# Kernel optimization log

Hardware: AMD Instinct MI355X
Metric: run time of the kernel (lower is better)

The kernel has to match this reference:

```python
import jax, jax.numpy as jnp
import numpy as np

B, S, HID = 2, 2048, 4096
H, P, N, G, K = 128, 64, 128, 8, 4      # heads, head_dim, ssm_state, groups, conv kernel
INTER = H * P                           # 8192
CONV_DIM = INTER + 2 * G * N            # 10240
CHUNK = 128
EPS = 1e-5
DT_MIN, DT_MAX = 0.0, 100.0


def setup_inputs() -> dict:
    key = jax.random.key(0)
    ks = jax.random.split(key, 4)
    proj = INTER + CONV_DIM + H
    return {
        "x": jax.random.normal(ks[0], (B, S, HID), jnp.float32),
        "in_proj_w": jax.random.normal(ks[1], (proj, HID), jnp.float32) * 0.02,
        "conv_w": jax.random.normal(ks[2], (CONV_DIM, 1, K), jnp.float32) * 0.2,
        "conv_b": jnp.zeros((CONV_DIM,), jnp.float32),
        "dt_bias": jnp.ones((H,), jnp.float32),
        "A_log": jnp.log(jnp.arange(1, H + 1, dtype=jnp.float32)),
        "D": jnp.ones((H,), jnp.float32),
        "norm_w": jnp.ones((INTER,), jnp.float32),
        "out_proj_w": jax.random.normal(ks[3], (HID, INTER), jnp.float32) * 0.02,
    }


def _segsum(a):
    # a: (..., c) -> (..., c, c); [i, j] = sum_{k=j+1..i} a[k] for i >= j, else -inf
    c = a.shape[-1]
    s = jnp.cumsum(a, axis=-1)
    diff = s[..., :, None] - s[..., None, :]
    mask = jnp.tril(jnp.ones((c, c), dtype=bool))
    return jnp.where(mask, diff, -jnp.inf)


def reference(x, in_proj_w, conv_w, conv_b, dt_bias, A_log, D, norm_w, out_proj_w):
    b, s, _ = x.shape
    proj = jnp.einsum('bsd,ed->bse', x, in_proj_w)
    gate = proj[..., :INTER]
    hBC = proj[..., INTER:INTER + CONV_DIM]
    dt = proj[..., INTER + CONV_DIM:]                       # (b, s, H)

    # depthwise causal conv1d + silu
    xc = jnp.transpose(hBC, (0, 2, 1))                      # (b, conv_dim, s)
    xc = jax.lax.conv_general_dilated(xc, conv_w, (1,), [(K - 1, 0)],
                                      dimension_numbers=('NCH', 'OIH', 'NCH'),
                                      feature_group_count=CONV_DIM)
    xc = xc + conv_b[None, :, None]
    hBC = jax.nn.silu(jnp.transpose(xc, (0, 2, 1)))

    hs = hBC[..., :INTER].reshape(b, s, H, P)
    Bm = hBC[..., INTER:INTER + G * N].reshape(b, s, G, N)
    Cm = hBC[..., INTER + G * N:].reshape(b, s, G, N)

    A = -jnp.exp(A_log)                                     # (H,)
    dt = jnp.clip(jax.nn.softplus(dt + dt_bias), DT_MIN, DT_MAX)

    rep = H // G
    Bh = jnp.repeat(Bm, rep, axis=2)                        # (b, s, H, N)
    Ch = jnp.repeat(Cm, rep, axis=2)

    nc = s // CHUNK
    xch = (hs * dt[..., None]).reshape(b, nc, CHUNK, H, P)  # dt-scaled input, chunked
    Bc = Bh.reshape(b, nc, CHUNK, H, N)
    Cc = Ch.reshape(b, nc, CHUNK, H, N)
    A_dt = (dt * A).reshape(b, nc, CHUNK, H).transpose(0, 3, 1, 2)  # (b, H, nc, c)
    A_cum = jnp.cumsum(A_dt, axis=-1)

    # intra-chunk (diagonal) contribution
    L = jnp.exp(_segsum(A_dt))                              # (b, H, nc, c, c)
    Y_diag = jnp.einsum('bzlhn,bzshn,bhzls,bzshp->bzlhp', Cc, Bc, L, xch)

    # per-chunk final states
    decay_states = jnp.exp(A_cum[..., -1:] - A_cum)         # (b, H, nc, c)
    states = jnp.einsum('bzlhn,bhzl,bzlhp->bzhpn', Bc, decay_states, xch)

    # inter-chunk recurrence (initial state = 0)
    states_p = jnp.concatenate([jnp.zeros_like(states[:, :1]), states], axis=1)  # (b, nc+1, H, P, N)
    A_last = jnp.pad(A_cum[..., -1], ((0, 0), (0, 0), (1, 0)))                   # (b, H, nc+1)
    decay_chunk = jnp.exp(_segsum(A_last))                                        # (b, H, nc+1, nc+1)
    new_states = jnp.einsum('bhzc,bchpn->bzhpn', decay_chunk, states_p)
    prev = new_states[:, :-1]                                # state entering each chunk

    Y_off = jnp.einsum('bzlhn,bzhpn,bhzl->bzlhp', Cc, prev, jnp.exp(A_cum))
    Y = (Y_diag + Y_off).reshape(b, s, H, P) + hs * D[None, None, :, None]
    y = Y.reshape(b, s, INTER)

    # gated grouped RMSNorm (norm_before_gate=False)
    g = y * jax.nn.silu(gate)
    gg = g.reshape(b, s, G, INTER // G)
    var = jnp.mean(gg * gg, axis=-1, keepdims=True)
    gg = gg * jax.lax.rsqrt(var + EPS)
    out = gg.reshape(b, s, INTER) * norm_w

    return jnp.einsum('bsi,oi->bso', out, out_proj_w)
```

## Files before the change

### kernel.cpp

```cpp
#include <hip/hip_runtime.h>
#include <hip/hip_bf16.h>
#include <cstdint>
#include <cstddef>

#define DEVI __device__ __forceinline__

#define BB 2
#define S_LEN 2048
#define HID_DIM 4096
#define NH 128
#define PD 64
#define NS 128
#define NG 8
#define INTER 8192
#define CONVD 10240
#define PROJ 18560
#define PROJP 18688
#define NC 16
#define BS 4096
#define GN 1024

using short8 = __attribute__((ext_vector_type(8))) short;
using short4v = __attribute__((ext_vector_type(4))) short;
using f32x4  = __attribute__((ext_vector_type(4))) float;
using bf16x8 = __attribute__((ext_vector_type(8))) __bf16;

DEVI float bf2f(short u) {
  union { unsigned int i; float f; } v;
  v.i = ((unsigned int)(unsigned short)u) << 16;
  return v.f;
}
DEVI short f2bf(float f) {
  union { float ff; unsigned int i; } v; v.ff = f;
  unsigned int x = v.i;
  return (short)((x + 0x7fffu + ((x >> 16) & 1u)) >> 16);
}
DEVI f32x4 mfma16(short8 a, short8 b, f32x4 c) {
  return __builtin_amdgcn_mfma_f32_16x16x32_bf16(
      __builtin_bit_cast(bf16x8, a), __builtin_bit_cast(bf16x8, b), c, 0, 0, 0);
}
DEVI void gl_lds16(const short* g, short* l) {
  __builtin_amdgcn_global_load_lds(
      (const __attribute__((address_space(1))) void*)g,
      (__attribute__((address_space(3))) void*)l, 16, 0, 0);
}
DEVI float sigmoidf_(float x) { return 1.f / (1.f + __expf(-x)); }

__global__ __launch_bounds__(256) void cvt_f32_bf16_k(const float* __restrict__ in,
                                                      short* __restrict__ out, size_t n) {
  size_t i = ((size_t)blockIdx.x * 256 + threadIdx.x) * 8;
  if (i + 8 > n) return;
  float4 a = *(const float4*)(in + i);
  float4 b = *(const float4*)(in + i + 4);
  short8 o;
  o[0] = f2bf(a.x); o[1] = f2bf(a.y); o[2] = f2bf(a.z); o[3] = f2bf(a.w);
  o[4] = f2bf(b.x); o[5] = f2bf(b.y); o[6] = f2bf(b.z); o[7] = f2bf(b.w);
  *(short8*)(out + i) = o;
}


#define STG(ISB, BUF, KH, TILE) do { \
  const short* _src = (ISB) ? Bt : A; \
  const int _r0 = (ISB) ? n0 : m0; \
  short* _lb = lds_ + ((ISB) ? 32768 : 0) + ((BUF)*2+(KH))*8192; \
  const int _kt = (TILE)*64 + (KH)*32; \
  { int _row = (wid*2)*16 + srow; int _sl = sps ^ ((_row>>1)&3); \
    gl_lds16(_src + (size_t)(_r0+_row)*K + _kt + _sl*8, _lb + (wid*2)*512); } \
  { int _row = (wid*2+1)*16 + srow; int _sl = sps ^ ((_row>>1)&3); \
    gl_lds16(_src + (size_t)(_r0+_row)*K + _kt + _sl*8, _lb + (wid*2+1)*512); } \
} while(0)

#define NOPS ((void)0)
#define VM6 asm volatile("s_waitcnt vmcnt(6)" ::: "memory")
#define VM0 asm volatile("s_waitcnt vmcnt(0)" ::: "memory")

#define LDAF(DST, BUF, KH, MIH) do { \
  _Pragma("unroll") \
  for (int _m = 0; _m < 4; ++_m) { \
    int _row = wr*128 + ((MIH)*4+_m)*16 + fr; \
    DST[_m] = *(const short8*)(lds_ + ((BUF)*2+(KH))*8192 + _row*32 + ((slot ^ ((_row>>1)&3))<<3)); \
  } \
} while(0)

#define LDBF(DST, BUF, KH) do { \
  _Pragma("unroll") \
  for (int _n = 0; _n < 4; ++_n) { \
    int _row = wc*64 + _n*16 + fr; \
    DST[_n] = *(const short8*)(lds_ + 32768 + ((BUF)*2+(KH))*8192 + _row*32 + ((slot ^ ((_row>>1)&3))<<3)); \
  } \
} while(0)

#define PH2(CAF, CBF, MIH, PFEN, PFAF, PFBF, PFB, PFKH, PFMIH, PFDOB, STGS, VMW) do { \
  STGS; VMW; \
  __builtin_amdgcn_s_barrier(); \
  if (PFEN) { LDAF(PFAF, PFB, PFKH, PFMIH); if (PFDOB) LDBF(PFBF, PFB, PFKH); } \
  __builtin_amdgcn_s_setprio(1); \
  _Pragma("unroll") \
  for (int _m = 0; _m < 4; ++_m) \
    _Pragma("unroll") \
    for (int _n = 0; _n < 4; ++_n) \
      acc[(MIH)*4+_m][_n] = mfma16(CAF[_m], CBF[_n], acc[(MIH)*4+_m][_n]); \
  __builtin_amdgcn_s_setprio(0); \
  asm volatile("s_waitcnt lgkmcnt(0)" ::: "memory"); \
  __builtin_amdgcn_sched_barrier(0); \
  __builtin_amdgcn_s_barrier(); \
} while(0)

template<int CB16>
__global__ __launch_bounds__(512, 2) void gemm256_k(const short* __restrict__ A,
                                                    const short* __restrict__ Bt,
                                                    void* __restrict__ Cout,
                                                    int Nstride, int K, int ntn) {
  __shared__ short lds_[65536];
  const int tid = threadIdx.x, wid = tid >> 6, lane = tid & 63;
  const int nwg = gridDim.x, orig = blockIdx.x;
  const int swz = (orig & 7) * (nwg >> 3) + (orig >> 3);
  const int per_group = ntn << 3;
  const int group = swz / per_group;
  const int rem = swz - group * per_group;
  const int m0 = (group * 8 + (rem & 7)) * 256;
  const int n0 = (rem >> 3) * 256;
  const int wr = wid >> 2, wc = wid & 3;
  const int fr = lane & 15, slot = lane >> 4;
  const int srow = lane >> 2, sps = lane & 3;

  f32x4 acc[8][4] = {};
  short8 af_a[4], af_b[4], bf_a[4], bf_b[4];
  const int NT = K >> 6;

  STG(1, 0, 0, 0); STG(0, 0, 0, 0); STG(1, 0, 1, 0); STG(0, 0, 1, 0);
  asm volatile("s_waitcnt vmcnt(4)" ::: "memory");
  STG(1, 1, 0, 1); STG(0, 1, 0, 1); STG(1, 1, 1, 1);
  asm volatile("s_waitcnt vmcnt(6)" ::: "memory");
  __builtin_amdgcn_s_barrier();
  LDAF(af_a, 0, 0, 0); LDBF(bf_a, 0, 0);
  asm volatile("s_waitcnt lgkmcnt(0)" ::: "memory");
  __builtin_amdgcn_sched_barrier(0);

  for (int i = 0; i < (NT >> 1) - 1; ++i) {
    const int t = 2 * i;
    PH2(af_a, bf_a, 0, 1, af_b, bf_a, 0, 0, 1, 0, STG(0, 1, 1, t + 1), NOPS);
    PH2(af_b, bf_a, 1, 1, af_a, bf_b, 0, 1, 0, 1, STG(1, 0, 0, t + 2), NOPS);
    PH2(af_a, bf_b, 0, 1, af_b, bf_a, 0, 1, 1, 0, STG(0, 0, 0, t + 2), NOPS);
    PH2(af_b, bf_b, 1, 1, af_a, bf_a, 1, 0, 0, 1, STG(1, 0, 1, t + 2), VM6);
    PH2(af_a, bf_a, 0, 1, af_b, bf_b, 1, 0, 1, 0, STG(0, 0, 1, t + 2), NOPS);
    PH2(af_b, bf_a, 1, 1, af_a, bf_b, 1, 1, 0, 1, STG(1, 1, 0, t + 3), NOPS);
    PH2(af_a, bf_b, 0, 1, af_b, bf_a, 1, 1, 1, 0, STG(0, 1, 0, t + 3), NOPS);
    PH2(af_b, bf_b, 1, 1, af_a, bf_a, 0, 0, 0, 1, STG(1, 1, 1, t + 3), VM6);
  }
  PH2(af_a, bf_a, 0, 1, af_b, bf_a, 0, 0, 1, 0, STG(0, 1, 1, NT - 1), NOPS);
  PH2(af_b, bf_a, 1, 1, af_a, bf_b, 0, 1, 0, 1, NOPS, NOPS);
  PH2(af_a, bf_b, 0, 1, af_b, bf_a, 0, 1, 1, 0, NOPS, NOPS);
  PH2(af_b, bf_b, 1, 1, af_a, bf_a, 1, 0, 0, 1, NOPS, VM0);
  PH2(af_a, bf_a, 0, 1, af_b, bf_b, 1, 0, 1, 0, NOPS, NOPS);
  PH2(af_b, bf_a, 1, 1, af_a, bf_b, 1, 1, 0, 1, NOPS, NOPS);
  PH2(af_a, bf_b, 0, 1, af_b, bf_a, 1, 1, 1, 0, NOPS, NOPS);
  PH2(af_b, bf_b, 1, 0, af_a, bf_a, 0, 0, 0, 0, NOPS, NOPS);

  const int er = (lane >> 4) * 4, ec = lane & 15;
  if (CB16) {
    short* C = (short*)Cout;
#pragma unroll
    for (int mi = 0; mi < 8; ++mi)
#pragma unroll
      for (int j = 0; j < 4; ++j) {
        size_t base = (size_t)(m0 + wr * 128 + mi * 16 + er + j) * Nstride + n0 + wc * 64 + ec;
#pragma unroll
        for (int ni = 0; ni < 4; ++ni) C[base + ni * 16] = f2bf(acc[mi][ni][j]);
      }
  } else {
    float* C = (float*)Cout;
#pragma unroll
    for (int mi = 0; mi < 8; ++mi)
#pragma unroll
      for (int j = 0; j < 4; ++j) {
        size_t base = (size_t)(m0 + wr * 128 + mi * 16 + er + j) * Nstride + n0 + wc * 64 + ec;
#pragma unroll
        for (int ni = 0; ni < 4; ++ni) C[base + ni * 16] = acc[mi][ni][j];
      }
  }
}

__global__ __launch_bounds__(256) void conv_silu_k(const short* __restrict__ projb,
                                                   const float* __restrict__ convw,
                                                   const float* __restrict__ convb,
                                                   short* __restrict__ hbc) {
  const int c = blockIdx.x * 256 + threadIdx.x;
  const int s0 = blockIdx.y * 256;
  const int b = blockIdx.z;
  const size_t rb = (size_t)b * S_LEN;
  const float* wp = convw + (size_t)c * 4;
  const float w0 = wp[0], w1 = wp[1], w2 = wp[2], w3 = wp[3];
  const float bias = convb[c];
  const short* pcol = projb + INTER + c;
  float x1 = 0.f, x2 = 0.f, x3 = 0.f;
  if (s0 > 0) {
    x3 = bf2f(pcol[(rb + s0 - 3) * PROJP]);
    x2 = bf2f(pcol[(rb + s0 - 2) * PROJP]);
    x1 = bf2f(pcol[(rb + s0 - 1) * PROJP]);
  }
  for (int s = s0; s < s0 + 256; ++s) {
    float v = bf2f(pcol[(rb + s) * PROJP]);
    float acc = bias + w0 * x3 + w1 * x2 + w2 * x1 + w3 * v;
    float o = acc * sigmoidf_(acc);
    hbc[(rb + s) * CONVD + c] = f2bf(o);
    x3 = x2; x2 = x1; x1 = v;
  }
}

__global__ __launch_bounds__(128) void acum_k(const short* __restrict__ projb,
                                              const float* __restrict__ dt_bias,
                                              const float* __restrict__ A_log,
                                              float* __restrict__ dtT,
                                              float* __restrict__ acum) {
  const int l = threadIdx.x;
  const int z = blockIdx.x, h = blockIdx.y, b = blockIdx.z;
  const float A = -__expf(A_log[h]);
  __shared__ float sv[128];
  const int r = b * S_LEN + z * 128 + l;
  float xv = bf2f(projb[(size_t)r * PROJP + INTER + CONVD + h]) + dt_bias[h];
  float sp = (xv > 20.f) ? xv : log1pf(__expf(xv));
  sp = fminf(fmaxf(sp, 0.f), 100.f);
  const size_t base = ((size_t)(b * NH + h)) * S_LEN + z * 128;
  dtT[base + l] = sp;
  sv[l] = sp * A;
  __syncthreads();
  for (int off = 1; off < 128; off <<= 1) {
    float t = (l >= off) ? sv[l - off] : 0.f;
    __syncthreads();
    sv[l] += t;
    __syncthreads();
  }
  acum[base + l] = sv[l];
}

__global__ __launch_bounds__(512) void states_k(const short* __restrict__ hbc,
                                                const float* __restrict__ dtT,
                                                const float* __restrict__ acum,
                                                float* __restrict__ states) {
  __shared__ short sBT[128 * 128];
  __shared__ short sxdt[64 * 128];
  const int tid = threadIdx.x, wid = tid >> 6, lane = tid & 63;
  const int g = blockIdx.x, z = blockIdx.y, b = blockIdx.z;
  const size_t srow0 = (size_t)(b * S_LEN + z * 128);
  const short* hrow = hbc + srow0 * CONVD;

  {
    const int l = tid & 127, n0b = (tid >> 7) * 32;
    const short* src = hrow + (size_t)l * CONVD + INTER + g * NS + n0b;
    short8 v0 = *(const short8*)(src);
    short8 v1 = *(const short8*)(src + 8);
    short8 v2 = *(const short8*)(src + 16);
    short8 v3 = *(const short8*)(src + 24);
#pragma unroll
    for (int j = 0; j < 8; ++j) {
      sBT[(n0b + j) * 128 + l] = v0[j];
      sBT[(n0b + 8 + j) * 128 + l] = v1[j];
      sBT[(n0b + 16 + j) * 128 + l] = v2[j];
      sBT[(n0b + 24 + j) * 128 + l] = v3[j];
    }
  }

  const int fr = lane & 15, fk8 = (lane >> 4) * 8;
  const int er = (lane >> 4) * 4, ec = lane & 15;
  const int pband = (wid & 3) * 16, nhalf = (wid >> 2) * 64;
  const int s2 = tid & 63, p0w = (tid >> 6) * 8;
  unsigned int* sx32 = (unsigned int*)sxdt;

  for (int hh = 0; hh < 16; ++hh) {
    const int h = g * 16 + hh;
    const float* ac_g = acum + ((size_t)(b * NH + h)) * S_LEN + z * 128;
    const float* dts = dtT + ((size_t)(b * NH + h)) * S_LEN + z * 128;
    __syncthreads();
    {
      const float acL = ac_g[127];
      float dv0 = dts[2 * s2] * __expf(acL - ac_g[2 * s2]);
      float dv1 = dts[2 * s2 + 1] * __expf(acL - ac_g[2 * s2 + 1]);
      const short* rsrc = hrow + (size_t)(2 * s2) * CONVD + (size_t)h * PD + p0w;
      short8 r0 = *(const short8*)(rsrc);
      short8 r1 = *(const short8*)(rsrc + CONVD);
#pragma unroll
      for (int j = 0; j < 8; ++j) {
        unsigned int lo = (unsigned short)f2bf(bf2f(r0[j]) * dv0);
        unsigned int hi = (unsigned short)f2bf(bf2f(r1[j]) * dv1);
        sx32[(p0w + j) * 64 + s2] = lo | (hi << 16);
      }
    }
    __syncthreads();
    f32x4 st[4] = {};
#pragma unroll
    for (int kk = 0; kk < 4; ++kk) {
      short8 a = *(const short8*)(sxdt + (pband + fr) * 128 + kk * 32 + fk8);
#pragma unroll
      for (int ni = 0; ni < 4; ++ni) {
        short8 bb = *(const short8*)(sBT + (nhalf + ni * 16 + fr) * 128 + kk * 32 + fk8);
        st[ni] = mfma16(a, bb, st[ni]);
      }
    }
    float* stp = states + (((size_t)(b * NC + z)) * NH + h) * (size_t)(NS * PD);
#pragma unroll
    for (int ni = 0; ni < 4; ++ni)
#pragma unroll
      for (int j = 0; j < 4; ++j)
        stp[(pband + er + j) * NS + nhalf + ni * 16 + ec] = st[ni][j];
  }
}

__global__ __launch_bounds__(256) void scan_k(float* __restrict__ states,
                                              const float* __restrict__ acum) {
  const int h = blockIdx.x, b = blockIdx.y;
  const int tid = threadIdx.x;
  float* stp = states + ((size_t)(b * NC * NH) + h) * (size_t)(NS * PD);
  const size_t cst = (size_t)NH * NS * PD;
  const float* ac = acum + ((size_t)(b * NH + h)) * S_LEN;
  float E[32];
#pragma unroll
  for (int i = 0; i < 32; ++i) E[i] = 0.f;
  const int n = tid & 127, pg = tid >> 7;
  for (int zz = 0; zz < NC; ++zz) {
    float* sz = stp + (size_t)zz * cst;
    short* pvb = (short*)sz;
    float tmp[32];
#pragma unroll
    for (int i = 0; i < 32; ++i) tmp[i] = sz[i * 256 + tid];
    __syncthreads();
    float dec = __expf(ac[zz * 128 + 127]);
#pragma unroll
    for (int i = 0; i < 32; ++i) {
      int p = i * 2 + pg;
      pvb[p * 128 + n] = f2bf(E[i]);
      E[i] = dec * E[i] + tmp[i];
    }
    __syncthreads();
  }
}

__global__ __launch_bounds__(512) void yfull_k(const short* __restrict__ hbc,
                                               const short* __restrict__ projb,
                                               const float* __restrict__ dtT,
                                               const float* __restrict__ acum,
                                               const float* __restrict__ states,
                                               const float* __restrict__ Dv,
                                               const float* __restrict__ norm_w,
                                               short* __restrict__ normed) {
  __shared__ short lds[50176];
  __shared__ float sac[128];
  __shared__ float sScale[128];
  __shared__ float sNW[1024];
  short* sC = lds;
  short* sB = lds + 16384;
  short* sxdt = lds + 16384;
  short* sprev = lds + 16384 + 8192;
  const int tid = threadIdx.x, wid = tid >> 6, lane = tid & 63;
  short* sPw = lds + 32768 + wid * 2176;
  const int g = blockIdx.x, z = blockIdx.y, b = blockIdx.z;
  const size_t srow0 = (size_t)(b * S_LEN + z * 128);
  const short* hrow = hbc + srow0 * CONVD;

  {
    const int n0_ = (lane & 15) * 8;
#pragma unroll
    for (int it = 0; it < 4; ++it) {
      int s = it * 32 + wid * 4 + (lane >> 4);
      gl_lds16(hrow + (size_t)s * CONVD + INTER + GN + g * NS + n0_, sC + (it * 32 + wid * 4) * 128);
      gl_lds16(hrow + (size_t)s * CONVD + INTER + g * NS + n0_, sB + (it * 32 + wid * 4) * 128);
    }
  }
  for (int i = tid; i < 1024; i += 512) sNW[i] = norm_w[g * 1024 + i];
  __syncthreads();

  const int fr = lane & 15, fk8 = (lane >> 4) * 8;
  const int er = (lane >> 4) * 4, ec = lane & 15;
  const int lrow = wid * 16;
  const int s2 = tid & 63, p0w = (tid >> 6) * 8;
  unsigned int* sx32 = (unsigned int*)sxdt;

  f32x4 sc[8] = {};
#pragma unroll
  for (int kk = 0; kk < 4; ++kk) {
    short8 a = *(const short8*)(sC + (lrow + fr) * 128 + kk * 32 + fk8);
#pragma unroll
    for (int si = 0; si < 8; ++si) {
      short8 bv = *(const short8*)(sB + (si * 16 + fr) * 128 + kk * 32 + fk8);
      sc[si] = mfma16(a, bv, sc[si]);
    }
  }

  float rssq[4] = {0.f, 0.f, 0.f, 0.f};

  for (int hh = 0; hh < 16; ++hh) {
    const int h = g * 16 + hh;
    const float* ac = acum + ((size_t)(b * NH + h)) * S_LEN + z * 128;
    const float* dts = dtT + ((size_t)(b * NH + h)) * S_LEN + z * 128;
    const short* pvb = (const short*)(states + (((size_t)(b * NC + z)) * NH + h) * (size_t)(NS * PD));
    __syncthreads();
    if (tid < 128) sac[tid] = ac[tid];
    {
      float dv0 = dts[2 * s2], dv1 = dts[2 * s2 + 1];
      const short* rsrc = hrow + (size_t)(2 * s2) * CONVD + (size_t)h * PD + p0w;
      short8 r0 = *(const short8*)(rsrc);
      short8 r1 = *(const short8*)(rsrc + CONVD);
#pragma unroll
      for (int j = 0; j < 8; ++j) {
        unsigned int lo = (unsigned short)f2bf(bf2f(r0[j]) * dv0);
        unsigned int hi = (unsigned short)f2bf(bf2f(r1[j]) * dv1);
        sx32[(p0w + j) * 64 + s2] = lo | (hi << 16);
      }
    }
    gl_lds16(pvb + wid * 1024 + lane * 8, sprev + wid * 1024);
    gl_lds16(pvb + wid * 1024 + 512 + lane * 8, sprev + wid * 1024 + 512);
    __syncthreads();

    {
      float acS[8];
#pragma unroll
      for (int si = 0; si < 8; ++si) acS[si] = sac[si * 16 + ec];
#pragma unroll
      for (int j = 0; j < 4; ++j) {
        int lloc = er + j;
        float acl = sac[lrow + lloc];
#pragma unroll
        for (int si = 0; si < 8; ++si) {
          int s = si * 16 + ec;
          float v = (s <= lrow + lloc) ? sc[si][j] * __expf(acl - acS[si]) : 0.f;
          sPw[lloc * 136 + s] = f2bf(v);
        }
      }
    }
    f32x4 yd[4] = {}, yo[4] = {};
#pragma unroll
    for (int kk = 0; kk < 4; ++kk) {
      short8 ap = *(const short8*)(sPw + fr * 136 + kk * 32 + fk8);
      short8 acf = *(const short8*)(sC + (lrow + fr) * 128 + kk * 32 + fk8);
#pragma unroll
      for (int ni = 0; ni < 4; ++ni) {
        short8 bv = *(const short8*)(sxdt + (ni * 16 + fr) * 128 + kk * 32 + fk8);
        yd[ni] = mfma16(ap, bv, yd[ni]);
        short8 bp = *(const short8*)(sprev + (ni * 16 + fr) * 128 + kk * 32 + fk8);
        yo[ni] = mfma16(acf, bp, yo[ni]);
      }
    }
    const float Dh = Dv[h];
#pragma unroll
    for (int j = 0; j < 4; ++j) {
      int l = lrow + er + j;
      float e_ac = __expf(sac[l]);
#pragma unroll
      for (int ni = 0; ni < 4; ++ni) {
        int p = ni * 16 + ec;
        float hs = bf2f(hrow[(size_t)l * CONVD + (size_t)h * PD + p]);
        float y = yd[ni][j] + yo[ni][j] * e_ac + hs * Dh;
        float gate = bf2f(projb[(srow0 + l) * (size_t)PROJP + (size_t)h * PD + p]);
        float gg = y * gate * sigmoidf_(gate);
        normed[(srow0 + l) * (size_t)INTER + (size_t)h * PD + p] = f2bf(gg);
        rssq[j] += gg * gg;
      }
    }
  }

#pragma unroll
  for (int j = 0; j < 4; ++j) {
#pragma unroll
    for (int m = 1; m <= 8; m <<= 1) rssq[j] += __shfl_xor(rssq[j], m, 64);
  }
  if (ec == 0) {
#pragma unroll
    for (int j = 0; j < 4; ++j) sScale[lrow + er + j] = rsqrtf(rssq[j] * (1.f / 1024.f) + 1e-5f);
  }
  __syncthreads();

  for (int e = tid * 8; e < 128 * 1024; e += 4096) {
    int row = e >> 10, ch = e & 1023;
    short* gp = normed + (srow0 + row) * (size_t)INTER + g * 1024 + ch;
    short8 gv = *(const short8*)(gp);
    float scl = sScale[row];
    short8 o;
#pragma unroll
    for (int q = 0; q < 8; ++q) o[q] = f2bf(bf2f(gv[q]) * scl * sNW[ch + q]);
    *(short8*)(gp) = o;
  }
}

extern "C" void kernel_launch(void* const* d_in, const int* in_sizes, int n_in,
                              void* d_out, int out_size, void* d_ws, size_t ws_size,
                              hipStream_t stream) {
  const float* x     = (const float*)d_in[0];
  const float* w1    = (const float*)d_in[1];
  const float* convw = (const float*)d_in[2];
  const float* convb = (const float*)d_in[3];
  const float* dtb   = (const float*)d_in[4];
  const float* alog  = (const float*)d_in[5];
  const float* Dv    = (const float*)d_in[6];
  const float* nw    = (const float*)d_in[7];
  const float* w2    = (const float*)d_in[8];
  float* out = (float*)d_out;

  char* ws = (char*)d_ws;
  size_t off = 0;
  float* dtT = (float*)(ws + off);  off += (size_t)BB * NH * S_LEN * 4;
  float* acum = (float*)(ws + off); off += (size_t)BB * NH * S_LEN * 4;
  short* xb = (short*)(ws + off);   off += (size_t)BS * HID_DIM * 2;
  char* w1region = ws + off;        off += (size_t)PROJP * HID_DIM * 2;
  short* w1b = (short*)w1region;
  short* normed = (short*)w1region;
  short* w2b = (short*)(w1region + (size_t)BS * INTER * 2);
  short* projb = (short*)(ws + off); off += (size_t)BS * PROJP * 2;
  short* hbc = (short*)(ws + off);   off += (size_t)BS * CONVD * 2;
  float* states = (float*)(ws + off); off += (size_t)BB * NC * NH * NS * PD * 4;

  const size_t nx = (size_t)BS * HID_DIM;
  const size_t nw1 = (size_t)PROJ * HID_DIM;
  const size_t nw2 = (size_t)HID_DIM * INTER;

  cvt_f32_bf16_k<<<dim3(nx / 2048), 256, 0, stream>>>(x, xb, nx);
  cvt_f32_bf16_k<<<dim3(nw1 / 2048), 256, 0, stream>>>(w1, w1b, nw1);

  gemm256_k<1><<<dim3(16 * 73), 512, 0, stream>>>(xb, w1b, projb, PROJP, HID_DIM, 73);

  cvt_f32_bf16_k<<<dim3(nw2 / 2048), 256, 0, stream>>>(w2, w2b, nw2);

  conv_silu_k<<<dim3(CONVD / 256, S_LEN / 256, BB), 256, 0, stream>>>(projb, convw, convb, hbc);
  acum_k<<<dim3(NC, NH, BB), 128, 0, stream>>>(projb, dtb, alog, dtT, acum);

  states_k<<<dim3(NG, NC, BB), 512, 0, stream>>>(hbc, dtT, acum, states);
  scan_k<<<dim3(NH, BB), 256, 0, stream>>>(states, acum);
  yfull_k<<<dim3(NG, NC, BB), 512, 0, stream>>>(hbc, projb, dtT, acum, states, Dv, nw, normed);

  gemm256_k<0><<<dim3(16 * 16), 512, 0, stream>>>(normed, w2b, out, HID_DIM, INTER, 16);
}
```

Baseline: 1.250 ms.

## Double-buffer per-head staging and swizzle LDS in states and y kernels

In states_k and yfull_k, the global loads for the next head (x*dt, acum, dt, prev states) are issued into registers before the current head's MFMA work. They are then written into the alternate LDS buffer afterward, which drops one barrier per head and overlaps load latency with compute. LDS layouts are padded (stride 136) or XOR-swizzled to reduce bank conflicts, and acum values move from shared memory into registers. The cost is more LDS (yfull grows to about 133KB) and higher register pressure, which could lower occupancy.

```diff
diff --git a/kernel.cpp b/kernel.cpp
--- a/kernel.cpp
+++ b/kernel.cpp
@@ -57,7 +57,6 @@
   o[4] = f2bf(b.x); o[5] = f2bf(b.y); o[6] = f2bf(b.z); o[7] = f2bf(b.w);
   *(short8*)(out + i) = o;
 }
-
 
 #define STG(ISB, BUF, KH, TILE) do { \
   const short* _src = (ISB) ? Bt : A; \
@@ -238,8 +237,8 @@
                                                 const float* __restrict__ dtT,
                                                 const float* __restrict__ acum,
                                                 float* __restrict__ states) {
-  __shared__ short sBT[128 * 128];
-  __shared__ short sxdt[64 * 128];
+  __shared__ short sBT[128 * 136];
+  __shared__ short sxdt2[2][64 * 136];
   const int tid = threadIdx.x, wid = tid >> 6, lane = tid & 63;
   const int g = blockIdx.x, z = blockIdx.y, b = blockIdx.z;
   const size_t srow0 = (size_t)(b * S_LEN + z * 128);
@@ -254,10 +253,10 @@
     short8 v3 = *(const short8*)(src + 24);
 #pragma unroll
     for (int j = 0; j < 8; ++j) {
-      sBT[(n0b + j) * 128 + l] = v0[j];
-      sBT[(n0b + 8 + j) * 128 + l] = v1[j];
-      sBT[(n0b + 16 + j) * 128 + l] = v2[j];
-      sBT[(n0b + 24 + j) * 128 + l] = v3[j];
+      sBT[(n0b + j) * 136 + l] = v0[j];
+      sBT[(n0b + 8 + j) * 136 + l] = v1[j];
+      sBT[(n0b + 16 + j) * 136 + l] = v2[j];
+      sBT[(n0b + 24 + j) * 136 + l] = v3[j];
     }
   }
 
@@ -265,35 +264,52 @@
   const int er = (lane >> 4) * 4, ec = lane & 15;
   const int pband = (wid & 3) * 16, nhalf = (wid >> 2) * 64;
   const int s2 = tid & 63, p0w = (tid >> 6) * 8;
-  unsigned int* sx32 = (unsigned int*)sxdt;
+
+  float cdv0, cdv1; short8 cr0, cr1;
+  {
+    const int h = g * 16;
+    const float* acg = acum + ((size_t)(b * NH + h)) * S_LEN + z * 128;
+    const float* dts = dtT + ((size_t)(b * NH + h)) * S_LEN + z * 128;
+    const float acL = acg[127];
+    cdv0 = dts[2 * s2] * __expf(acL - acg[2 * s2]);
+    cdv1 = dts[2 * s2 + 1] * __expf(acL - acg[2 * s2 + 1]);
+    const short* rsrc = hrow + (size_t)(2 * s2) * CONVD + (size_t)h * PD + p0w;
+    cr0 = *(const short8*)(rsrc);
+    cr1 = *(const short8*)(rsrc + CONVD);
+  }
+  {
+    unsigned int* x32 = (unsigned int*)sxdt2[0];
+#pragma unroll
+    for (int j = 0; j < 8; ++j) {
+      unsigned int lo = (unsigned short)f2bf(bf2f(cr0[j]) * cdv0);
+      unsigned int hi = (unsigned short)f2bf(bf2f(cr1[j]) * cdv1);
+      x32[(p0w + j) * 68 + s2] = lo | (hi << 16);
+    }
+  }
+  __syncthreads();
 
   for (int hh = 0; hh < 16; ++hh) {
     const int h = g * 16 + hh;
-    const float* ac_g = acum + ((size_t)(b * NH + h)) * S_LEN + z * 128;
-    const float* dts = dtT + ((size_t)(b * NH + h)) * S_LEN + z * 128;
-    __syncthreads();
-    {
-      const float acL = ac_g[127];
-      float dv0 = dts[2 * s2] * __expf(acL - ac_g[2 * s2]);
-      float dv1 = dts[2 * s2 + 1] * __expf(acL - ac_g[2 * s2 + 1]);
-      const short* rsrc = hrow + (size_t)(2 * s2) * CONVD + (size_t)h * PD + p0w;
-      short8 r0 = *(const short8*)(rsrc);
-      short8 r1 = *(const short8*)(rsrc + CONVD);
-#pragma unroll
-      for (int j = 0; j < 8; ++j) {
-        unsigned int lo = (unsigned short)f2bf(bf2f(r0[j]) * dv0);
-        unsigned int hi = (unsigned short)f2bf(bf2f(r1[j]) * dv1);
-        sx32[(p0w + j) * 64 + s2] = lo | (hi << 16);
-      }
-    }
-    __syncthreads();
+    float ndv0 = 0.f, ndv1 = 0.f; short8 nr0, nr1;
+    if (hh < 15) {
+      const int h2 = h + 1;
+      const float* acg = acum + ((size_t)(b * NH + h2)) * S_LEN + z * 128;
+      const float* dts = dtT + ((size_t)(b * NH + h2)) * S_LEN + z * 128;
+      const float acL = acg[127];
+      ndv0 = dts[2 * s2] * __expf(acL - acg[2 * s2]);
+      ndv1 = dts[2 * s2 + 1] * __expf(acL - acg[2 * s2 + 1]);
+      const short* rsrc = hrow + (size_t)(2 * s2) * CONVD + (size_t)h2 * PD + p0w;
+      nr0 = *(const short8*)(rsrc);
+      nr1 = *(const short8*)(rsrc + CONVD);
+    }
+    const short* sx = sxdt2[hh & 1];
     f32x4 st[4] = {};
 #pragma unroll
     for (int kk = 0; kk < 4; ++kk) {
-      short8 a = *(const short8*)(sxdt + (pband + fr) * 128 + kk * 32 + fk8);
+      short8 a = *(const short8*)(sx + (pband + fr) * 136 + kk * 32 + fk8);
 #pragma unroll
       for (int ni = 0; ni < 4; ++ni) {
-        short8 bb = *(const short8*)(sBT + (nhalf + ni * 16 + fr) * 128 + kk * 32 + fk8);
+        short8 bb = *(const short8*)(sBT + (nhalf + ni * 16 + fr) * 136 + kk * 32 + fk8);
         st[ni] = mfma16(a, bb, st[ni]);
       }
     }
@@ -303,6 +319,16 @@
 #pragma unroll
       for (int j = 0; j < 4; ++j)
         stp[(pband + er + j) * NS + nhalf + ni * 16 + ec] = st[ni][j];
+    if (hh < 15) {
+      unsigned int* x32 = (unsigned int*)sxdt2[(hh + 1) & 1];
+#pragma unroll
+      for (int j = 0; j < 8; ++j) {
+        unsigned int lo = (unsigned short)f2bf(bf2f(nr0[j]) * ndv0);
+        unsigned int hi = (unsigned short)f2bf(bf2f(nr1[j]) * ndv1);
+        x32[(p0w + j) * 68 + s2] = lo | (hi << 16);
+      }
+    }
+    __syncthreads();
   }
 }
 
@@ -335,6 +361,39 @@
   }
 }
 
+#define RDSW(BUF, ROWBASE, KK) \
+  (*(const short8*)((BUF) + ((ROWBASE) + fr) * 128 + ((((KK) * 4 + slot4) ^ sw7) << 3)))
+
+#define WRX(DST, D0, D1, R0, R1) do { \
+  unsigned int* _x = (unsigned int*)(DST); \
+  _Pragma("unroll") \
+  for (int _j = 0; _j < 8; ++_j) { \
+    unsigned int _lo = (unsigned short)f2bf(bf2f(R0[_j]) * (D0)); \
+    unsigned int _hi = (unsigned short)f2bf(bf2f(R1[_j]) * (D1)); \
+    _x[(p0w + _j) * 64 + ((((s2 >> 2) ^ _j) << 2) | (s2 & 3))] = _lo | (_hi << 16); \
+  } \
+} while (0)
+
+#define WRP(DST, P0, P1) do { \
+  int _p = tid >> 3; int _s0 = (tid & 7) * 2; int _m = _p & 7; \
+  *(short8*)((DST) + _p * 128 + ((_s0 ^ _m) << 3)) = P0; \
+  *(short8*)((DST) + _p * 128 + (((_s0 + 1) ^ _m) << 3)) = P1; \
+} while (0)
+
+#define LOADH_Y(H, DT0, DT1, ACS, ACL, R0, R1, P0, P1) do { \
+  const float* _ac = acum + ((size_t)(b * NH + (H))) * S_LEN + z * 128; \
+  const float* _dts = dtT + ((size_t)(b * NH + (H))) * S_LEN + z * 128; \
+  DT0 = _dts[2 * s2]; DT1 = _dts[2 * s2 + 1]; \
+  _Pragma("unroll") \
+  for (int _si = 0; _si < 8; ++_si) ACS[_si] = _ac[_si * 16 + ec]; \
+  _Pragma("unroll") \
+  for (int _j = 0; _j < 4; ++_j) ACL[_j] = _ac[lrow + er + _j]; \
+  const short* _rs = hrow + (size_t)(2 * s2) * CONVD + (size_t)(H) * PD + p0w; \
+  R0 = *(const short8*)(_rs); R1 = *(const short8*)(_rs + CONVD); \
+  const short* _pv = (const short*)(states + (((size_t)(b * NC + z)) * NH + (H)) * (size_t)(NS * PD)); \
+  P0 = *(const short8*)(_pv + tid * 16); P1 = *(const short8*)(_pv + tid * 16 + 8); \
+} while (0)
+
 __global__ __launch_bounds__(512) void yfull_k(const short* __restrict__ hbc,
                                                const short* __restrict__ projb,
                                                const float* __restrict__ dtT,
@@ -343,22 +402,22 @@
                                                const float* __restrict__ Dv,
                                                const float* __restrict__ norm_w,
                                                short* __restrict__ normed) {
-  __shared__ short lds[50176];
-  __shared__ float sac[128];
+  __shared__ short lds[66560];
   __shared__ float sScale[128];
   __shared__ float sNW[1024];
   short* sC = lds;
   short* sB = lds + 16384;
-  short* sxdt = lds + 16384;
-  short* sprev = lds + 16384 + 8192;
+  short* sx0 = lds + 32768;
+  short* sp0 = lds + 40960;
   const int tid = threadIdx.x, wid = tid >> 6, lane = tid & 63;
-  short* sPw = lds + 32768 + wid * 2176;
+  short* sPw = lds + 49152 + wid * 2176;
   const int g = blockIdx.x, z = blockIdx.y, b = blockIdx.z;
   const size_t srow0 = (size_t)(b * S_LEN + z * 128);
   const short* hrow = hbc + srow0 * CONVD;
 
   {
-    const int n0_ = (lane & 15) * 8;
+    const int slot_g = (lane & 15) ^ (((wid & 1) << 2) | (lane >> 4));
+    const int n0_ = slot_g * 8;
 #pragma unroll
     for (int it = 0; it < 4; ++it) {
       int s = it * 32 + wid * 4 + (lane >> 4);
@@ -370,73 +429,61 @@
   __syncthreads();
 
   const int fr = lane & 15, fk8 = (lane >> 4) * 8;
+  const int slot4 = lane >> 4, sw7 = lane & 7;
   const int er = (lane >> 4) * 4, ec = lane & 15;
   const int lrow = wid * 16;
   const int s2 = tid & 63, p0w = (tid >> 6) * 8;
-  unsigned int* sx32 = (unsigned int*)sxdt;
+
+  float cdt0, cdt1, cacS[8], cacl[4];
+  short8 cr0, cr1, cp0, cp1;
+  LOADH_Y(g * 16, cdt0, cdt1, cacS, cacl, cr0, cr1, cp0, cp1);
 
   f32x4 sc[8] = {};
 #pragma unroll
   for (int kk = 0; kk < 4; ++kk) {
-    short8 a = *(const short8*)(sC + (lrow + fr) * 128 + kk * 32 + fk8);
+    short8 a = RDSW(sC, lrow, kk);
 #pragma unroll
     for (int si = 0; si < 8; ++si) {
-      short8 bv = *(const short8*)(sB + (si * 16 + fr) * 128 + kk * 32 + fk8);
+      short8 bv = RDSW(sB, si * 16, kk);
       sc[si] = mfma16(a, bv, sc[si]);
     }
   }
+  WRX(sx0, cdt0, cdt1, cr0, cr1);
+  WRP(sp0, cp0, cp1);
+  __syncthreads();
 
   float rssq[4] = {0.f, 0.f, 0.f, 0.f};
 
   for (int hh = 0; hh < 16; ++hh) {
     const int h = g * 16 + hh;
-    const float* ac = acum + ((size_t)(b * NH + h)) * S_LEN + z * 128;
-    const float* dts = dtT + ((size_t)(b * NH + h)) * S_LEN + z * 128;
-    const short* pvb = (const short*)(states + (((size_t)(b * NC + z)) * NH + h) * (size_t)(NS * PD));
-    __syncthreads();
-    if (tid < 128) sac[tid] = ac[tid];
-    {
-      float dv0 = dts[2 * s2], dv1 = dts[2 * s2 + 1];
-      const short* rsrc = hrow + (size_t)(2 * s2) * CONVD + (size_t)h * PD + p0w;
-      short8 r0 = *(const short8*)(rsrc);
-      short8 r1 = *(const short8*)(rsrc + CONVD);
-#pragma unroll
-      for (int j = 0; j < 8; ++j) {
-        unsigned int lo = (unsigned short)f2bf(bf2f(r0[j]) * dv0);
-        unsigned int hi = (unsigned short)f2bf(bf2f(r1[j]) * dv1);
-        sx32[(p0w + j) * 64 + s2] = lo | (hi << 16);
-      }
-    }
-    gl_lds16(pvb + wid * 1024 + lane * 8, sprev + wid * 1024);
-    gl_lds16(pvb + wid * 1024 + 512 + lane * 8, sprev + wid * 1024 + 512);
-    __syncthreads();
-
-    {
-      float acS[8];
-#pragma unroll
-      for (int si = 0; si < 8; ++si) acS[si] = sac[si * 16 + ec];
-#pragma unroll
-      for (int j = 0; j < 4; ++j) {
-        int lloc = er + j;
-        float acl = sac[lrow + lloc];
-#pragma unroll
-        for (int si = 0; si < 8; ++si) {
-          int s = si * 16 + ec;
-          float v = (s <= lrow + lloc) ? sc[si][j] * __expf(acl - acS[si]) : 0.f;
-          sPw[lloc * 136 + s] = f2bf(v);
-        }
+    float ndt0 = 0.f, ndt1 = 0.f, nacS[8], nacl[4];
+    short8 nr0, nr1, np0, np1;
+    if (hh < 15) LOADH_Y(h + 1, ndt0, ndt1, nacS, nacl, nr0, nr1, np0, np1);
+
+    short* sx = (hh & 1) ? sB : sx0;
+    short* sp = (hh & 1) ? (sB + 8192) : sp0;
+
+#pragma unroll
+    for (int j = 0; j < 4; ++j) {
+      int lloc = er + j;
+      float acl = cacl[j];
+#pragma unroll
+      for (int si = 0; si < 8; ++si) {
+        int sI = si * 16 + ec;
+        float v = (sI <= lrow + lloc) ? sc[si][j] * __expf(acl - cacS[si]) : 0.f;
+        sPw[lloc * 136 + sI] = f2bf(v);
       }
     }
     f32x4 yd[4] = {}, yo[4] = {};
 #pragma unroll
     for (int kk = 0; kk < 4; ++kk) {
       short8 ap = *(const short8*)(sPw + fr * 136 + kk * 32 + fk8);
-      short8 acf = *(const short8*)(sC + (lrow + fr) * 128 + kk * 32 + fk8);
+      short8 acf = RDSW(sC, lrow, kk);
 #pragma unroll
       for (int ni = 0; ni < 4; ++ni) {
-        short8 bv = *(const short8*)(sxdt + (ni * 16 + fr) * 128 + kk * 32 + fk8);
+        short8 bv = RDSW(sx, ni * 16, kk);
         yd[ni] = mfma16(ap, bv, yd[ni]);
-        short8 bp = *(const short8*)(sprev + (ni * 16 + fr) * 128 + kk * 32 + fk8);
+        short8 bp = RDSW(sp, ni * 16, kk);
         yo[ni] = mfma16(acf, bp, yo[ni]);
       }
     }
@@ -444,7 +491,7 @@
 #pragma unroll
     for (int j = 0; j < 4; ++j) {
       int l = lrow + er + j;
-      float e_ac = __expf(sac[l]);
+      float e_ac = __expf(cacl[j]);
 #pragma unroll
       for (int ni = 0; ni < 4; ++ni) {
         int p = ni * 16 + ec;
@@ -456,6 +503,18 @@
         rssq[j] += gg * gg;
       }
     }
+    if (hh < 15) {
+      short* nx = (hh & 1) ? sx0 : sB;
+      short* npv = (hh & 1) ? sp0 : (sB + 8192);
+      WRX(nx, ndt0, ndt1, nr0, nr1);
+      WRP(npv, np0, np1);
+      cdt0 = ndt0; cdt1 = ndt1; cr0 = nr0; cr1 = nr1; cp0 = np0; cp1 = np1;
+#pragma unroll
+      for (int si = 0; si < 8; ++si) cacS[si] = nacS[si];
+#pragma unroll
+      for (int j = 0; j < 4; ++j) cacl[j] = nacl[j];
+    }
+    __syncthreads();
   }
 
 #pragma unroll
```

Measured after the change: 1.183 ms. -5.4%, faster.
